# Kernel tuning notes

Hardware: AMD Instinct MI355X
Metric: run time of the kernel (lower is better)

## Reference

```python
import jax, jax.numpy as jnp
import numpy as np

# Faithful JAX port of MultiHeadSelfAttention.forward.
# Key observations about the torch code:
#  * einsum 'abcdef,ghdefi->abcdefi' with g=h=1 is a broadcast multiply:
#      U_hat_I[a,b,c,d,e,f,i] = U_hat[a,b,c,d,e,f] * W_affine[0,0,d,e,f,i]
#  * The per-i matmul loop builds A[...,e,e',i], but the follow-up einsum
#    'abcdeeg,abcdefg->abcdefg' only reads the DIAGONAL of A, i.e.
#      diag[...,e,i] = sum_f U_hat_I[...,e,f,i]^2 / sqrt(dim_capsules)
#    so we compute the diagonal directly (same math, no e x e intermediate).
#  * A_ = diag (broadcast over f) * W_t, then softmax over the f axis (dim=-2).

def setup_inputs() -> dict:
    key = jax.random.key(0)
    k1, k2, k3 = jax.random.split(key, 3)
    B, S1, S2, NC, DC, F, I = 32, 14, 14, 2, 16, 32, 8
    U_hat = jax.random.normal(k1, (B, S1, S2, NC, DC, F), dtype=jnp.float32)
    W_t = jax.random.normal(k2, (1, NC, DC, F, I), dtype=jnp.float32)
    W_affine = jax.random.normal(k3, (1, 1, NC, DC, F, I), dtype=jnp.float32)
    return {"U_hat": U_hat, "W_t": W_t, "W_affine": W_affine}


def reference(U_hat, W_t, W_affine):
    dim_capsules = U_hat.shape[4]
    d = jnp.sqrt(jnp.asarray(dim_capsules, dtype=U_hat.dtype))
    # (B,S1,S2,nc,dc,f,1) * (nc,dc,f,I) -> (B,S1,S2,nc,dc,f,I)
    U_hat_I = U_hat[..., None] * W_affine[0, 0]
    # diagonal of A_i = (X X^T)/sqrt(d): row-wise squared norm over f
    diag = jnp.sum(U_hat_I * U_hat_I, axis=-2) / d  # (B,S1,S2,nc,dc,I)
    # A_[a,b,c,d,e,f,i] = diag[a,b,c,d,e,i] * W_t[0,d,e,f,i]
    A_ = diag[..., None, :] * W_t[0]  # (B,S1,S2,nc,dc,f,I)
    C = jax.nn.softmax(A_, axis=-2)  # softmax over f (dim=-2)
    return (C, U_hat_I)
```

## Files before the change

### kernel.cpp

```cpp
#include <hip/hip_runtime.h>

#define N_ROWS     200704
#define F_DIM      32
#define I_DIM      8
#define ROW_ELEMS  256
#define C_ELEMS    51380224LL
#define WAVES_PER_BLOCK 4

__global__ __launch_bounds__(256) void mhsa_softmax_kernel(
    const float* __restrict__ U_hat,
    const float* __restrict__ W_t,
    const float* __restrict__ W_affine,
    float* __restrict__ out)
{
    const int wave = threadIdx.x >> 6;
    const int lane = threadIdx.x & 63;
    const int r    = blockIdx.x * WAVES_PER_BLOCK + wave;
    const int fg = lane >> 3;
    const int de = r & 31;

    const float* uh   = U_hat    + (long long)r * F_DIM;
    const float* wa   = W_affine + de * ROW_ELEMS;
    const float* wt   = W_t      + de * ROW_ELEMS;
    float*       outC = out      + (long long)r * ROW_ELEMS;
    float*       outU = out + C_ELEMS + (long long)r * ROW_ELEMS;

    float u[4], wav[4], wtv[4], uhi[4];
#pragma unroll
    for (int j = 0; j < 4; ++j) {
        u[j]   = uh[fg + 8 * j];
        wav[j] = wa[64 * j + lane];
        wtv[j] = wt[64 * j + lane];
    }

    float sq = 0.f;
#pragma unroll
    for (int j = 0; j < 4; ++j) {
        uhi[j] = u[j] * wav[j];
        outU[64 * j + lane] = uhi[j];
        sq = fmaf(uhi[j], uhi[j], sq);
    }
    sq += __shfl_xor(sq, 8);
    sq += __shfl_xor(sq, 16);
    sq += __shfl_xor(sq, 32);
    const float diag = sq * 0.25f;

    float a[4];
    float m = -INFINITY;
#pragma unroll
    for (int j = 0; j < 4; ++j) {
        a[j] = diag * wtv[j];
        m = fmaxf(m, a[j]);
    }
    m = fmaxf(m, __shfl_xor(m, 8));
    m = fmaxf(m, __shfl_xor(m, 16));
    m = fmaxf(m, __shfl_xor(m, 32));

    float e[4], s = 0.f;
#pragma unroll
    for (int j = 0; j < 4; ++j) {
        e[j] = __expf(a[j] - m);
        s += e[j];
    }
    s += __shfl_xor(s, 8);
    s += __shfl_xor(s, 16);
    s += __shfl_xor(s, 32);
    const float inv = 1.0f / s;

#pragma unroll
    for (int j = 0; j < 4; ++j) {
        outC[64 * j + lane] = e[j] * inv;
    }
}

extern "C" void kernel_launch(void* const* d_in, const int* in_sizes, int n_in,
                              void* d_out, int out_size, void* d_ws, size_t ws_size,
                              hipStream_t stream) {
    const float* U_hat    = (const float*)d_in[0];
    const float* W_t      = (const float*)d_in[1];
    const float* W_affine = (const float*)d_in[2];
    float* out = (float*)d_out;

    const int grid = N_ROWS / WAVES_PER_BLOCK;
    mhsa_softmax_kernel<<<grid, 256, 0, stream>>>(U_hat, W_t, W_affine, out);
}
```

Baseline: 442.3 us.

## Make softmax kernel persistent, hoist per-wave weights and precompute max

Switches from one wave per row to a fixed grid of 2048 blocks whose waves loop over rows with a grid stride. The stride is a multiple of 32, so each wave's W_affine/W_t slice stays the same and is loaded once. Because the squared-norm diag is non-negative, the row max is computed once as diag times the max of W_t, which drops one cross-lane reduction per row. The division is replaced by a hardware reciprocal. In exchange, each wave works through its rows one after another, so fewer memory requests may be in flight per CU.

```diff
diff --git a/kernel.cpp b/kernel.cpp
--- a/kernel.cpp
+++ b/kernel.cpp
@@ -1,11 +1,11 @@
 #include <hip/hip_runtime.h>
 
-#define N_ROWS     200704
-#define F_DIM      32
-#define I_DIM      8
-#define ROW_ELEMS  256
-#define C_ELEMS    51380224LL
+#define N_ROWS      200704
+#define ROW_ELEMS   256
+#define C_ELEMS     51380224LL
+#define BLOCKS      2048
 #define WAVES_PER_BLOCK 4
+#define TOTAL_WAVES (BLOCKS * WAVES_PER_BLOCK)
 
 __global__ __launch_bounds__(256) void mhsa_softmax_kernel(
     const float* __restrict__ U_hat,
@@ -13,63 +13,60 @@
     const float* __restrict__ W_affine,
     float* __restrict__ out)
 {
-    const int wave = threadIdx.x >> 6;
     const int lane = threadIdx.x & 63;
-    const int r    = blockIdx.x * WAVES_PER_BLOCK + wave;
+    const int wid  = blockIdx.x * WAVES_PER_BLOCK + (threadIdx.x >> 6);
     const int fg = lane >> 3;
-    const int de = r & 31;
+    const int de = wid & 31;
 
-    const float* uh   = U_hat    + (long long)r * F_DIM;
-    const float* wa   = W_affine + de * ROW_ELEMS;
-    const float* wt   = W_t      + de * ROW_ELEMS;
-    float*       outC = out      + (long long)r * ROW_ELEMS;
-    float*       outU = out + C_ELEMS + (long long)r * ROW_ELEMS;
+    const float* wa = W_affine + de * ROW_ELEMS;
+    const float* wt = W_t      + de * ROW_ELEMS;
 
-    float u[4], wav[4], wtv[4], uhi[4];
+    float wav[4], wtv[4];
 #pragma unroll
     for (int j = 0; j < 4; ++j) {
-        u[j]   = uh[fg + 8 * j];
         wav[j] = wa[64 * j + lane];
         wtv[j] = wt[64 * j + lane];
     }
+    float wtmax = fmaxf(fmaxf(wtv[0], wtv[1]), fmaxf(wtv[2], wtv[3]));
+    wtmax = fmaxf(wtmax, __shfl_xor(wtmax, 8));
+    wtmax = fmaxf(wtmax, __shfl_xor(wtmax, 16));
+    wtmax = fmaxf(wtmax, __shfl_xor(wtmax, 32));
 
-    float sq = 0.f;
+    for (int r = wid; r < N_ROWS; r += TOTAL_WAVES) {
+        const float* uh   = U_hat + (long long)r * 32;
+        float*       outC = out   + (long long)r * ROW_ELEMS;
+        float*       outU = out + C_ELEMS + (long long)r * ROW_ELEMS;
+
+        float u[4], uhi[4];
 #pragma unroll
-    for (int j = 0; j < 4; ++j) {
-        uhi[j] = u[j] * wav[j];
-        outU[64 * j + lane] = uhi[j];
-        sq = fmaf(uhi[j], uhi[j], sq);
-    }
-    sq += __shfl_xor(sq, 8);
-    sq += __shfl_xor(sq, 16);
-    sq += __shfl_xor(sq, 32);
-    const float diag = sq * 0.25f;
+        for (int j = 0; j < 4; ++j) u[j] = uh[fg + 8 * j];
 
-    float a[4];
-    float m = -INFINITY;
+        float sq = 0.f;
 #pragma unroll
-    for (int j = 0; j < 4; ++j) {
-        a[j] = diag * wtv[j];
-        m = fmaxf(m, a[j]);
-    }
-    m = fmaxf(m, __shfl_xor(m, 8));
-    m = fmaxf(m, __shfl_xor(m, 16));
-    m = fmaxf(m, __shfl_xor(m, 32));
+        for (int j = 0; j < 4; ++j) {
+            uhi[j] = u[j] * wav[j];
+            outU[64 * j + lane] = uhi[j];
+            sq = fmaf(uhi[j], uhi[j], sq);
+        }
+        sq += __shfl_xor(sq, 8);
+        sq += __shfl_xor(sq, 16);
+        sq += __shfl_xor(sq, 32);
+        const float diag = sq * 0.25f;
+        const float m    = diag * wtmax;
 
-    float e[4], s = 0.f;
+        float e[4], s = 0.f;
 #pragma unroll
-    for (int j = 0; j < 4; ++j) {
-        e[j] = __expf(a[j] - m);
-        s += e[j];
-    }
-    s += __shfl_xor(s, 8);
-    s += __shfl_xor(s, 16);
-    s += __shfl_xor(s, 32);
-    const float inv = 1.0f / s;
+        for (int j = 0; j < 4; ++j) {
+            e[j] = __expf(fmaf(diag, wtv[j], -m));
+            s += e[j];
+        }
+        s += __shfl_xor(s, 8);
+        s += __shfl_xor(s, 16);
+        s += __shfl_xor(s, 32);
+        const float inv = __builtin_amdgcn_rcpf(s);
 
 #pragma unroll
-    for (int j = 0; j < 4; ++j) {
-        outC[64 * j + lane] = e[j] * inv;
+        for (int j = 0; j < 4; ++j) outC[64 * j + lane] = e[j] * inv;
     }
 }
 
@@ -81,6 +78,5 @@
     const float* W_affine = (const float*)d_in[2];
     float* out = (float*)d_out;
 
-    const int grid = N_ROWS / WAVES_PER_BLOCK;
-    mhsa_softmax_kernel<<<grid, 256, 0, stream>>>(U_hat, W_t, W_affine, out);
+    mhsa_softmax_kernel<<<BLOCKS, 256, 0, stream>>>(U_hat, W_t, W_affine, out);
 }
```

New measurement: 436.6 us. Within noise of the previous version (-1.3%).
